# Performance work log

Measured on AMD Instinct MI355X. Metric: run time of the kernel, lower is better.

The kernel has to match this reference:

```python
import jax, jax.numpy as jnp
import numpy as np

B, S, E, H = 2, 2048, 512, 8
HD = E // H  # head dim = 64


def setup_inputs() -> dict:
    key = jax.random.key(0)
    k1, k2, k3 = jax.random.split(key, 3)
    scale_qkv = (6.0 / (E + 3 * E)) ** 0.5  # xavier-uniform-like scale
    scale_o = (6.0 / (E + E)) ** 0.5
    return {
        "X": jax.random.normal(k1, (B, S, E), dtype=jnp.float32),
        "Wqkv": jax.random.uniform(k2, (E, 3 * E), jnp.float32, -scale_qkv, scale_qkv),
        "bqkv": jnp.zeros((3 * E,), jnp.float32),
        "Wo": jax.random.uniform(k3, (E, E), jnp.float32, -scale_o, scale_o),
        "bo": jnp.zeros((E,), jnp.float32),
    }


def reference(X, Wqkv, bqkv, Wo, bo):
    b, s, e = X.shape
    # qkv projection: [B,S,3E] -> [B,S,H,3*HD] -> [B,H,S,3*HD]
    qkv = X @ Wqkv + bqkv
    qkv = qkv.reshape(b, s, H, 3 * HD).transpose(0, 2, 1, 3)
    q, k, v = jnp.array_split(qkv, 3, axis=-1)  # each [B,H,S,HD]
    # naive scaled dot-product attention (full score matrix, per source)
    attn_logits = jnp.einsum("bhqd,bhkd->bhqk", q, k) / jnp.sqrt(jnp.float32(HD))
    attention = jax.nn.softmax(attn_logits, axis=-1)  # [B,H,S,S]
    values = jnp.einsum("bhqk,bhkd->bhqd", attention, v)
    values = values.transpose(0, 2, 1, 3).reshape(b, s, e)
    o = values @ Wo + bo
    return (o, attention)
```

## Files before the change

### kernel.cpp

```cpp
#include <hip/hip_runtime.h>

typedef unsigned short u16;
typedef u16 u16x2 __attribute__((ext_vector_type(2)));
typedef u16 u16x4 __attribute__((ext_vector_type(4)));
typedef u16 u16x8 __attribute__((ext_vector_type(8)));
typedef __bf16 bf16x8 __attribute__((ext_vector_type(8)));
typedef float f32x4 __attribute__((ext_vector_type(4)));
typedef float f32x2 __attribute__((ext_vector_type(2)));

#define MFMA16(A, B, C) __builtin_amdgcn_mfma_f32_16x16x32_bf16(A, B, C, 0, 0, 0)

#define SB 2
#define SS 2048
#define SE 512
#define SH 8
#define SHD 64

__device__ __forceinline__ u16 f2b(float f) {
  union { float f; unsigned u; } v;
  v.f = f;
  unsigned r = v.u + 0x7FFFu + ((v.u >> 16) & 1u);
  return (u16)(r >> 16);
}

__device__ __forceinline__ bf16x8 as_bf16x8(u16x8 v) {
  return __builtin_bit_cast(bf16x8, v);
}

__global__ __launch_bounds__(256)
void convx_kernel(const float* __restrict__ X, u16* __restrict__ Xb)
{
  const int i = (blockIdx.x * 256 + threadIdx.x) * 4;
  const float4 v = *(const float4*)&X[i];
  u16x4 o;
  o[0] = f2b(v.x); o[1] = f2b(v.y); o[2] = f2b(v.z); o[3] = f2b(v.w);
  *(u16x4*)&Xb[i] = o;
}

__global__ __launch_bounds__(256)
void wtrans_kernel(const float* __restrict__ in, u16* __restrict__ out, int N)
{
  __shared__ float t[32][33];
  const int tid = threadIdx.x;
  const int r = tid >> 3, c4 = (tid & 7) * 4;
  const int k0 = blockIdx.y * 32, n0 = blockIdx.x * 32;
  const float4 v = *(const float4*)&in[(size_t)(k0 + r) * N + n0 + c4];
  t[r][c4 + 0] = v.x; t[r][c4 + 1] = v.y; t[r][c4 + 2] = v.z; t[r][c4 + 3] = v.w;
  __syncthreads();
  u16x4 o;
  o[0] = f2b(t[c4 + 0][r]);
  o[1] = f2b(t[c4 + 1][r]);
  o[2] = f2b(t[c4 + 2][r]);
  o[3] = f2b(t[c4 + 3][r]);
  *(u16x4*)&out[(n0 + r) * 512 + k0 + c4] = o;
}

template <int MODE>
__global__ __launch_bounds__(256, 2)
void gemm_kernel(const u16* __restrict__ A, const u16* __restrict__ Bt,
                 const float* __restrict__ bias,
                 u16* __restrict__ Q, u16* __restrict__ K, u16* __restrict__ Vt,
                 float* __restrict__ Out)
{
  __shared__ __align__(16) u16 As[128 * 40];
  __shared__ __align__(16) u16 Bs[128 * 40];
  const int tid  = threadIdx.x;
  const int lane = tid & 63, wave = tid >> 6, quad = lane >> 4, l16 = lane & 15;
  const int m0 = blockIdx.y * 128, n0 = blockIdx.x * 128;
  const int wr = (wave >> 1) * 64, wc = (wave & 1) * 64;
  const int sr = tid >> 2, sc = (tid & 3) * 8;

  const f32x4 z4 = {0.f, 0.f, 0.f, 0.f};
  f32x4 acc[4][4];
#pragma unroll
  for (int i = 0; i < 4; i++)
#pragma unroll
    for (int j = 0; j < 4; j++) acc[i][j] = z4;

  for (int k0 = 0; k0 < 512; k0 += 32) {
    const u16x8 a0 = *(const u16x8*)&A[(m0 + sr) * 512 + k0 + sc];
    const u16x8 a1 = *(const u16x8*)&A[(m0 + 64 + sr) * 512 + k0 + sc];
    const u16x8 b0 = *(const u16x8*)&Bt[(n0 + sr) * 512 + k0 + sc];
    const u16x8 b1 = *(const u16x8*)&Bt[(n0 + 64 + sr) * 512 + k0 + sc];
    __syncthreads();
    *(u16x8*)&As[sr * 40 + sc]        = a0;
    *(u16x8*)&As[(64 + sr) * 40 + sc] = a1;
    *(u16x8*)&Bs[sr * 40 + sc]        = b0;
    *(u16x8*)&Bs[(64 + sr) * 40 + sc] = b1;
    __syncthreads();
    bf16x8 af[4], bf[4];
#pragma unroll
    for (int i = 0; i < 4; i++) {
      af[i] = as_bf16x8(*(const u16x8*)&As[(wr + i * 16 + l16) * 40 + quad * 8]);
      bf[i] = as_bf16x8(*(const u16x8*)&Bs[(wc + i * 16 + l16) * 40 + quad * 8]);
    }
#pragma unroll
    for (int i = 0; i < 4; i++)
#pragma unroll
      for (int j = 0; j < 4; j++) acc[i][j] = MFMA16(af[i], bf[j], acc[i][j]);
  }

#pragma unroll
  for (int tm = 0; tm < 4; tm++) {
#pragma unroll
    for (int tn = 0; tn < 4; tn++) {
#pragma unroll
      for (int r = 0; r < 4; r++) {
        const int gm = m0 + wr + tm * 16 + quad * 4 + r;
        const int gn = n0 + wc + tn * 16 + l16;
        const float v = acc[tm][tn][r] + bias[gn];
        if (MODE == 0) {
          const int bb = gm >> 11, s = gm & 2047;
          const int hh = gn / 192, j = gn - hh * 192;
          const int bh = bb * SH + hh;
          if (j < 64)
            Q[(bh * SS + s) * SHD + j] = f2b(v * 0.125f);
          else if (j < 128)
            K[(bh * SS + s) * SHD + (j - 64)] = f2b(v);
          else
            Vt[(bh * SHD + (j - 128)) * SS + s] = f2b(v);
        } else {
          Out[gm * 512 + gn] = v;
        }
      }
    }
  }
}

__global__ __launch_bounds__(512, 2)
void attn_kernel(const u16* __restrict__ Q, const u16* __restrict__ K,
                 const u16* __restrict__ Vt, u16* __restrict__ values,
                 float* __restrict__ attn)
{
  __shared__ __align__(16) u16 p_lds[8 * 16 * 264];
  __shared__ float redmax[8][16];
  __shared__ float redsum[8][16];

  const int tid  = threadIdx.x;
  const int lane = tid & 63, wave = tid >> 6, quad = lane >> 4, l16 = lane & 15;
  const int q0 = blockIdx.x * 16;
  const int h = blockIdx.y, b = blockIdx.z, bh = b * SH + h;

  const u16* Qb = Q + bh * SS * SHD;
  const u16* Kb = K + bh * SS * SHD;
  const u16* Vb = Vt + bh * SHD * SS;

  const bf16x8 aq0 = as_bf16x8(*(const u16x8*)&Qb[(q0 + l16) * SHD + quad * 8]);
  const bf16x8 aq1 = as_bf16x8(*(const u16x8*)&Qb[(q0 + l16) * SHD + 32 + quad * 8]);

  f32x4 acc[16];
#pragma unroll
  for (int ct = 0; ct < 16; ct++) {
    const int kb = wave * 256 + ct * 16;
    bf16x8 bk0 = as_bf16x8(*(const u16x8*)&Kb[(kb + l16) * SHD + quad * 8]);
    bf16x8 bk1 = as_bf16x8(*(const u16x8*)&Kb[(kb + l16) * SHD + 32 + quad * 8]);
    f32x4 c = {0.f, 0.f, 0.f, 0.f};
    c = MFMA16(aq0, bk0, c);
    c = MFMA16(aq1, bk1, c);
    acc[ct] = c;
  }

  float mx[4];
#pragma unroll
  for (int r = 0; r < 4; r++) mx[r] = acc[0][r];
#pragma unroll
  for (int ct = 1; ct < 16; ct++)
#pragma unroll
    for (int r = 0; r < 4; r++) mx[r] = fmaxf(mx[r], acc[ct][r]);
#pragma unroll
  for (int off = 1; off < 16; off <<= 1)
#pragma unroll
    for (int r = 0; r < 4; r++) mx[r] = fmaxf(mx[r], __shfl_xor(mx[r], off));
  if (l16 == 0) {
#pragma unroll
    for (int r = 0; r < 4; r++) redmax[wave][quad * 4 + r] = mx[r];
  }
  __syncthreads();
  float gm[4];
#pragma unroll
  for (int r = 0; r < 4; r++) {
    float m = redmax[0][quad * 4 + r];
#pragma unroll
    for (int w = 1; w < 8; w++) m = fmaxf(m, redmax[w][quad * 4 + r]);
    gm[r] = m;
  }

  float ls[4] = {0.f, 0.f, 0.f, 0.f};
#pragma unroll
  for (int ct = 0; ct < 16; ct++)
#pragma unroll
    for (int r = 0; r < 4; r++) {
      const float p = __expf(acc[ct][r] - gm[r]);
      acc[ct][r] = p;
      ls[r] += p;
    }
#pragma unroll
  for (int off = 1; off < 16; off <<= 1)
#pragma unroll
    for (int r = 0; r < 4; r++) ls[r] += __shfl_xor(ls[r], off);
  if (l16 == 0) {
#pragma unroll
    for (int r = 0; r < 4; r++) redsum[wave][quad * 4 + r] = ls[r];
  }
  __syncthreads();
  float inv[4];
#pragma unroll
  for (int r = 0; r < 4; r++) {
    float s = redsum[0][quad * 4 + r];
#pragma unroll
    for (int w = 1; w < 8; w++) s += redsum[w][quad * 4 + r];
    inv[r] = 1.f / s;
  }

  float* attn_b = attn + (bh * SS + q0) * SS;
#pragma unroll
  for (int ct = 0; ct < 16; ct++) {
    const int col = wave * 256 + ct * 16 + l16;
#pragma unroll
    for (int r = 0; r < 4; r++) {
      const float p = acc[ct][r] * inv[r];
      attn_b[(quad * 4 + r) * SS + col] = p;
      p_lds[(wave * 16 + quad * 4 + r) * 264 + ct * 16 + l16] = f2b(p);
    }
  }

  f32x4 oacc[4];
#pragma unroll
  for (int nt = 0; nt < 4; nt++) oacc[nt] = (f32x4){0.f, 0.f, 0.f, 0.f};
#pragma unroll
  for (int kc = 0; kc < 8; kc++) {
    bf16x8 pa = as_bf16x8(*(const u16x8*)&p_lds[(wave * 16 + l16) * 264 + kc * 32 + quad * 8]);
    const int sb = wave * 256 + kc * 32 + quad * 8;
#pragma unroll
    for (int nt = 0; nt < 4; nt++) {
      bf16x8 vb = as_bf16x8(*(const u16x8*)&Vb[(nt * 16 + l16) * SS + sb]);
      oacc[nt] = MFMA16(pa, vb, oacc[nt]);
    }
  }

  __syncthreads();
  float* opart = (float*)p_lds;
#pragma unroll
  for (int nt = 0; nt < 4; nt++)
#pragma unroll
    for (int r = 0; r < 4; r++)
      opart[(wave * 16 + quad * 4 + r) * 64 + nt * 16 + l16] = oacc[nt][r];
  __syncthreads();

  const int q = tid >> 5, d0 = (tid & 31) * 2;
  f32x2 s2 = {0.f, 0.f};
#pragma unroll
  for (int w = 0; w < 8; w++) s2 += *(const f32x2*)&opart[(w * 16 + q) * 64 + d0];
  u16x2 o2;
  o2[0] = f2b(s2[0]);
  o2[1] = f2b(s2[1]);
  *(u16x2*)&values[((b * SS + q0 + q) * SH + h) * SHD + d0] = o2;
}

extern "C" void kernel_launch(void* const* d_in, const int* in_sizes, int n_in,
                              void* d_out, int out_size, void* d_ws, size_t ws_size,
                              hipStream_t stream) {
  const float* X    = (const float*)d_in[0];
  const float* Wqkv = (const float*)d_in[1];
  const float* bqkv = (const float*)d_in[2];
  const float* Wo   = (const float*)d_in[3];
  const float* bo   = (const float*)d_in[4];

  float* o_out    = (float*)d_out;
  float* attn_out = o_out + SB * SS * SE;

  const size_t QKV_ELEMS = (size_t)SB * SH * SS * SHD;
  u16* Q      = (u16*)d_ws;
  u16* K      = Q + QKV_ELEMS;
  u16* Vt     = K + QKV_ELEMS;
  u16* values = Vt + QKV_ELEMS;
  u16* Xb     = values;
  u16* WqkvT  = (u16*)attn_out;
  u16* WoT    = Q;

  convx_kernel<<<dim3(2048), 256, 0, stream>>>(X, Xb);
  wtrans_kernel<<<dim3(48, 16), 256, 0, stream>>>(Wqkv, WqkvT, 1536);

  gemm_kernel<0><<<dim3(12, 32), 256, 0, stream>>>(Xb, WqkvT, bqkv, Q, K, Vt, nullptr);
  attn_kernel<<<dim3(128, 8, 2), 512, 0, stream>>>(Q, K, Vt, values, attn_out);
  wtrans_kernel<<<dim3(16, 16), 256, 0, stream>>>(Wo, WoT, 512);
  gemm_kernel<1><<<dim3(4, 32), 256, 0, stream>>>(values, WoT, bo,
                                                  nullptr, nullptr, nullptr, o_out);
}
```

Measured before the change: 441.2 us.

## Restructure attention so each wave owns full query rows with two-pass online softmax

Each wave now handles 16 full query rows across all 2048 keys, instead of eight waves splitting the key range of one 16-row tile. It uses a first pass with online max/sum statistics and a second pass that recomputes QK^T to write probabilities and accumulate PV. This removes the cross-wave LDS reductions, block barriers and the partial-output reduction. The grid is remapped to 512 blocks of 256 threads with a swizzled block index for L2 locality, and the LDS stride is padded. The cost is recomputing QK^T twice and re-reading K per wave.

```diff
diff --git a/kernel.cpp b/kernel.cpp
--- a/kernel.cpp
+++ b/kernel.cpp
@@ -127,134 +127,122 @@
   }
 }
 
-__global__ __launch_bounds__(512, 2)
+#define PSTR 268
+
+__global__ __launch_bounds__(256, 2)
 void attn_kernel(const u16* __restrict__ Q, const u16* __restrict__ K,
                  const u16* __restrict__ Vt, u16* __restrict__ values,
                  float* __restrict__ attn)
 {
-  __shared__ __align__(16) u16 p_lds[8 * 16 * 264];
-  __shared__ float redmax[8][16];
-  __shared__ float redsum[8][16];
+  __shared__ __align__(16) u16 p_lds[4][16 * PSTR];
 
   const int tid  = threadIdx.x;
   const int lane = tid & 63, wave = tid >> 6, quad = lane >> 4, l16 = lane & 15;
-  const int q0 = blockIdx.x * 16;
-  const int h = blockIdx.y, b = blockIdx.z, bh = b * SH + h;
-
-  const u16* Qb = Q + bh * SS * SHD;
-  const u16* Kb = K + bh * SS * SHD;
-  const u16* Vb = Vt + bh * SHD * SS;
+
+  const int bid = blockIdx.x;
+  const int wg  = (bid & 7) * 64 + (bid >> 3);
+  const int qt  = wg & 31;
+  const int bh  = wg >> 5;
+  const int h = bh & 7, b = bh >> 3;
+  const int q0 = qt * 64 + wave * 16;
+
+  const u16* Qb = Q + (size_t)bh * SS * SHD;
+  const u16* Kb = K + (size_t)bh * SS * SHD;
+  const u16* Vb = Vt + (size_t)bh * SHD * SS;
 
   const bf16x8 aq0 = as_bf16x8(*(const u16x8*)&Qb[(q0 + l16) * SHD + quad * 8]);
   const bf16x8 aq1 = as_bf16x8(*(const u16x8*)&Qb[(q0 + l16) * SHD + 32 + quad * 8]);
 
-  f32x4 acc[16];
-#pragma unroll
-  for (int ct = 0; ct < 16; ct++) {
-    const int kb = wave * 256 + ct * 16;
-    bf16x8 bk0 = as_bf16x8(*(const u16x8*)&Kb[(kb + l16) * SHD + quad * 8]);
-    bf16x8 bk1 = as_bf16x8(*(const u16x8*)&Kb[(kb + l16) * SHD + 32 + quad * 8]);
-    f32x4 c = {0.f, 0.f, 0.f, 0.f};
-    c = MFMA16(aq0, bk0, c);
-    c = MFMA16(aq1, bk1, c);
-    acc[ct] = c;
-  }
-
-  float mx[4];
-#pragma unroll
-  for (int r = 0; r < 4; r++) mx[r] = acc[0][r];
-#pragma unroll
-  for (int ct = 1; ct < 16; ct++)
-#pragma unroll
-    for (int r = 0; r < 4; r++) mx[r] = fmaxf(mx[r], acc[ct][r]);
-#pragma unroll
-  for (int off = 1; off < 16; off <<= 1)
-#pragma unroll
-    for (int r = 0; r < 4; r++) mx[r] = fmaxf(mx[r], __shfl_xor(mx[r], off));
-  if (l16 == 0) {
-#pragma unroll
-    for (int r = 0; r < 4; r++) redmax[wave][quad * 4 + r] = mx[r];
-  }
-  __syncthreads();
-  float gm[4];
-#pragma unroll
-  for (int r = 0; r < 4; r++) {
-    float m = redmax[0][quad * 4 + r];
-#pragma unroll
-    for (int w = 1; w < 8; w++) m = fmaxf(m, redmax[w][quad * 4 + r]);
-    gm[r] = m;
-  }
-
-  float ls[4] = {0.f, 0.f, 0.f, 0.f};
-#pragma unroll
-  for (int ct = 0; ct < 16; ct++)
+  float m[4] = {-1e30f, -1e30f, -1e30f, -1e30f};
+  float l[4] = {0.f, 0.f, 0.f, 0.f};
+  for (int kt = 0; kt < 8; kt++) {
+    f32x4 acc[16];
+#pragma unroll
+    for (int ct = 0; ct < 16; ct++) {
+      const int kb = kt * 256 + ct * 16;
+      bf16x8 bk0 = as_bf16x8(*(const u16x8*)&Kb[(kb + l16) * SHD + quad * 8]);
+      bf16x8 bk1 = as_bf16x8(*(const u16x8*)&Kb[(kb + l16) * SHD + 32 + quad * 8]);
+      f32x4 c = {0.f, 0.f, 0.f, 0.f};
+      c = MFMA16(aq0, bk0, c);
+      c = MFMA16(aq1, bk1, c);
+      acc[ct] = c;
+    }
 #pragma unroll
     for (int r = 0; r < 4; r++) {
-      const float p = __expf(acc[ct][r] - gm[r]);
-      acc[ct][r] = p;
-      ls[r] += p;
-    }
-#pragma unroll
-  for (int off = 1; off < 16; off <<= 1)
-#pragma unroll
-    for (int r = 0; r < 4; r++) ls[r] += __shfl_xor(ls[r], off);
-  if (l16 == 0) {
-#pragma unroll
-    for (int r = 0; r < 4; r++) redsum[wave][quad * 4 + r] = ls[r];
-  }
-  __syncthreads();
+      float tm = acc[0][r];
+#pragma unroll
+      for (int ct = 1; ct < 16; ct++) tm = fmaxf(tm, acc[ct][r]);
+      const float mn = fmaxf(m[r], tm);
+      float s = 0.f;
+#pragma unroll
+      for (int ct = 0; ct < 16; ct++) s += __expf(acc[ct][r] - mn);
+      l[r] = l[r] * __expf(m[r] - mn) + s;
+      m[r] = mn;
+    }
+  }
+#pragma unroll
+  for (int off = 1; off < 16; off <<= 1) {
+#pragma unroll
+    for (int r = 0; r < 4; r++) {
+      const float m2 = __shfl_xor(m[r], off);
+      const float l2 = __shfl_xor(l[r], off);
+      const float mn = fmaxf(m[r], m2);
+      l[r] = l[r] * __expf(m[r] - mn) + l2 * __expf(m2 - mn);
+      m[r] = mn;
+    }
+  }
   float inv[4];
 #pragma unroll
-  for (int r = 0; r < 4; r++) {
-    float s = redsum[0][quad * 4 + r];
-#pragma unroll
-    for (int w = 1; w < 8; w++) s += redsum[w][quad * 4 + r];
-    inv[r] = 1.f / s;
-  }
-
-  float* attn_b = attn + (bh * SS + q0) * SS;
-#pragma unroll
-  for (int ct = 0; ct < 16; ct++) {
-    const int col = wave * 256 + ct * 16 + l16;
+  for (int r = 0; r < 4; r++) inv[r] = 1.f / l[r];
+
+  float* attn_b = attn + ((size_t)bh * SS + q0) * SS;
+  u16* pl = &p_lds[wave][0];
+  f32x4 oacc[4];
+#pragma unroll
+  for (int nt = 0; nt < 4; nt++) oacc[nt] = (f32x4){0.f, 0.f, 0.f, 0.f};
+
+  for (int kt = 0; kt < 8; kt++) {
+    f32x4 acc[16];
+#pragma unroll
+    for (int ct = 0; ct < 16; ct++) {
+      const int kb = kt * 256 + ct * 16;
+      bf16x8 bk0 = as_bf16x8(*(const u16x8*)&Kb[(kb + l16) * SHD + quad * 8]);
+      bf16x8 bk1 = as_bf16x8(*(const u16x8*)&Kb[(kb + l16) * SHD + 32 + quad * 8]);
+      f32x4 c = {0.f, 0.f, 0.f, 0.f};
+      c = MFMA16(aq0, bk0, c);
+      c = MFMA16(aq1, bk1, c);
+      acc[ct] = c;
+    }
+#pragma unroll
+    for (int ct = 0; ct < 16; ct++) {
+#pragma unroll
+      for (int r = 0; r < 4; r++) {
+        const float p = __expf(acc[ct][r] - m[r]) * inv[r];
+        attn_b[(quad * 4 + r) * SS + kt * 256 + ct * 16 + l16] = p;
+        pl[(quad * 4 + r) * PSTR + ct * 16 + l16] = f2b(p);
+      }
+    }
+#pragma unroll
+    for (int kc = 0; kc < 8; kc++) {
+      bf16x8 pa = as_bf16x8(*(const u16x8*)&pl[l16 * PSTR + kc * 32 + quad * 8]);
+      const int sb = kt * 256 + kc * 32 + quad * 8;
+#pragma unroll
+      for (int nt = 0; nt < 4; nt++) {
+        bf16x8 vb = as_bf16x8(*(const u16x8*)&Vb[(nt * 16 + l16) * SS + sb]);
+        oacc[nt] = MFMA16(pa, vb, oacc[nt]);
+      }
+    }
+  }
+
+#pragma unroll
+  for (int nt = 0; nt < 4; nt++) {
 #pragma unroll
     for (int r = 0; r < 4; r++) {
-      const float p = acc[ct][r] * inv[r];
-      attn_b[(quad * 4 + r) * SS + col] = p;
-      p_lds[(wave * 16 + quad * 4 + r) * 264 + ct * 16 + l16] = f2b(p);
-    }
-  }
-
-  f32x4 oacc[4];
-#pragma unroll
-  for (int nt = 0; nt < 4; nt++) oacc[nt] = (f32x4){0.f, 0.f, 0.f, 0.f};
-#pragma unroll
-  for (int kc = 0; kc < 8; kc++) {
-    bf16x8 pa = as_bf16x8(*(const u16x8*)&p_lds[(wave * 16 + l16) * 264 + kc * 32 + quad * 8]);
-    const int sb = wave * 256 + kc * 32 + quad * 8;
-#pragma unroll
-    for (int nt = 0; nt < 4; nt++) {
-      bf16x8 vb = as_bf16x8(*(const u16x8*)&Vb[(nt * 16 + l16) * SS + sb]);
-      oacc[nt] = MFMA16(pa, vb, oacc[nt]);
-    }
-  }
-
-  __syncthreads();
-  float* opart = (float*)p_lds;
-#pragma unroll
-  for (int nt = 0; nt < 4; nt++)
-#pragma unroll
-    for (int r = 0; r < 4; r++)
-      opart[(wave * 16 + quad * 4 + r) * 64 + nt * 16 + l16] = oacc[nt][r];
-  __syncthreads();
-
-  const int q = tid >> 5, d0 = (tid & 31) * 2;
-  f32x2 s2 = {0.f, 0.f};
-#pragma unroll
-  for (int w = 0; w < 8; w++) s2 += *(const f32x2*)&opart[(w * 16 + q) * 64 + d0];
-  u16x2 o2;
-  o2[0] = f2b(s2[0]);
-  o2[1] = f2b(s2[1]);
-  *(u16x2*)&values[((b * SS + q0 + q) * SH + h) * SHD + d0] = o2;
+      const int qrow = q0 + quad * 4 + r;
+      values[((size_t)(b * SS + qrow) * SH + h) * SHD + nt * 16 + l16] =
+          f2b(oacc[nt][r]);
+    }
+  }
 }
 
 extern "C" void kernel_launch(void* const* d_in, const int* in_sizes, int n_in,
@@ -282,7 +270,7 @@
   wtrans_kernel<<<dim3(48, 16), 256, 0, stream>>>(Wqkv, WqkvT, 1536);
 
   gemm_kernel<0><<<dim3(12, 32), 256, 0, stream>>>(Xb, WqkvT, bqkv, Q, K, Vt, nullptr);
-  attn_kernel<<<dim3(128, 8, 2), 512, 0, stream>>>(Q, K, Vt, values, attn_out);
+  attn_kernel<<<dim3(512), 256, 0, stream>>>(Q, K, Vt, values, attn_out);
   wtrans_kernel<<<dim3(16, 16), 256, 0, stream>>>(Wo, WoT, 512);
   gemm_kernel<1><<<dim3(4, 32), 256, 0, stream>>>(values, WoT, bo,
                                                   nullptr, nullptr, nullptr, o_out);
```

After: 474.7 us. 7.6% more time.

## Merge softmax max/sum reductions into one barrier with rescaling, nontemporal attn stores

Applied to the files above, without the earlier changes.

Each wave now computes a local max and local sum of exponentials before a single block barrier. The global max and sum are then combined online with exp rescaling, which replaces the previous two-barrier max-then-sum sequence. Per-wave LDS regions let the barrier before the partial-output writes be dropped, and the attention matrix is written with nontemporal stores to avoid polluting cache. Launch bounds are raised to 4 blocks per CU to push occupancy, which risks register spills since each thread holds 16 accumulator vectors.

```diff
diff --git a/kernel.cpp b/kernel.cpp
--- a/kernel.cpp
+++ b/kernel.cpp
@@ -127,23 +127,26 @@
   }
 }
 
-__global__ __launch_bounds__(512, 2)
+#define PSTR 264
+#define PWAVE (16 * PSTR)
+
+__global__ __launch_bounds__(512, 4)
 void attn_kernel(const u16* __restrict__ Q, const u16* __restrict__ K,
                  const u16* __restrict__ Vt, u16* __restrict__ values,
                  float* __restrict__ attn)
 {
-  __shared__ __align__(16) u16 p_lds[8 * 16 * 264];
-  __shared__ float redmax[8][16];
-  __shared__ float redsum[8][16];
+  __shared__ __align__(16) u16 p_lds[8 * PWAVE];
+  __shared__ float srm[8][16];
+  __shared__ float srl[8][16];
 
   const int tid  = threadIdx.x;
   const int lane = tid & 63, wave = tid >> 6, quad = lane >> 4, l16 = lane & 15;
   const int q0 = blockIdx.x * 16;
   const int h = blockIdx.y, b = blockIdx.z, bh = b * SH + h;
 
-  const u16* Qb = Q + bh * SS * SHD;
-  const u16* Kb = K + bh * SS * SHD;
-  const u16* Vb = Vt + bh * SHD * SS;
+  const u16* Qb = Q + (size_t)bh * SS * SHD;
+  const u16* Kb = K + (size_t)bh * SS * SHD;
+  const u16* Vb = Vt + (size_t)bh * SHD * SS;
 
   const bf16x8 aq0 = as_bf16x8(*(const u16x8*)&Qb[(q0 + l16) * SHD + quad * 8]);
   const bf16x8 aq1 = as_bf16x8(*(const u16x8*)&Qb[(q0 + l16) * SHD + 32 + quad * 8]);
@@ -160,67 +163,61 @@
     acc[ct] = c;
   }
 
-  float mx[4];
-#pragma unroll
-  for (int r = 0; r < 4; r++) mx[r] = acc[0][r];
-#pragma unroll
-  for (int ct = 1; ct < 16; ct++)
-#pragma unroll
-    for (int r = 0; r < 4; r++) mx[r] = fmaxf(mx[r], acc[ct][r]);
-#pragma unroll
-  for (int off = 1; off < 16; off <<= 1)
-#pragma unroll
-    for (int r = 0; r < 4; r++) mx[r] = fmaxf(mx[r], __shfl_xor(mx[r], off));
+  float mw[4], lw[4];
+#pragma unroll
+  for (int r = 0; r < 4; r++) {
+    float m = acc[0][r];
+#pragma unroll
+    for (int ct = 1; ct < 16; ct++) m = fmaxf(m, acc[ct][r]);
+#pragma unroll
+    for (int off = 1; off < 16; off <<= 1) m = fmaxf(m, __shfl_xor(m, off));
+    mw[r] = m;
+  }
+#pragma unroll
+  for (int r = 0; r < 4; r++) {
+    float s = 0.f;
+#pragma unroll
+    for (int ct = 0; ct < 16; ct++) {
+      const float p = __expf(acc[ct][r] - mw[r]);
+      acc[ct][r] = p;
+      s += p;
+    }
+#pragma unroll
+    for (int off = 1; off < 16; off <<= 1) s += __shfl_xor(s, off);
+    lw[r] = s;
+  }
   if (l16 == 0) {
 #pragma unroll
-    for (int r = 0; r < 4; r++) redmax[wave][quad * 4 + r] = mx[r];
+    for (int r = 0; r < 4; r++) {
+      srm[wave][quad * 4 + r] = mw[r];
+      srl[wave][quad * 4 + r] = lw[r];
+    }
   }
   __syncthreads();
-  float gm[4];
+
+  float scale[4];
 #pragma unroll
   for (int r = 0; r < 4; r++) {
-    float m = redmax[0][quad * 4 + r];
-#pragma unroll
-    for (int w = 1; w < 8; w++) m = fmaxf(m, redmax[w][quad * 4 + r]);
-    gm[r] = m;
-  }
-
-  float ls[4] = {0.f, 0.f, 0.f, 0.f};
-#pragma unroll
-  for (int ct = 0; ct < 16; ct++)
-#pragma unroll
-    for (int r = 0; r < 4; r++) {
-      const float p = __expf(acc[ct][r] - gm[r]);
-      acc[ct][r] = p;
-      ls[r] += p;
-    }
-#pragma unroll
-  for (int off = 1; off < 16; off <<= 1)
-#pragma unroll
-    for (int r = 0; r < 4; r++) ls[r] += __shfl_xor(ls[r], off);
-  if (l16 == 0) {
-#pragma unroll
-    for (int r = 0; r < 4; r++) redsum[wave][quad * 4 + r] = ls[r];
-  }
-  __syncthreads();
-  float inv[4];
-#pragma unroll
-  for (int r = 0; r < 4; r++) {
-    float s = redsum[0][quad * 4 + r];
-#pragma unroll
-    for (int w = 1; w < 8; w++) s += redsum[w][quad * 4 + r];
-    inv[r] = 1.f / s;
-  }
-
-  float* attn_b = attn + (bh * SS + q0) * SS;
+    const int row = quad * 4 + r;
+    float mg = srm[0][row];
+#pragma unroll
+    for (int w = 1; w < 8; w++) mg = fmaxf(mg, srm[w][row]);
+    float lg = 0.f;
+#pragma unroll
+    for (int w = 0; w < 8; w++) lg += srl[w][row] * __expf(srm[w][row] - mg);
+    scale[r] = __expf(mw[r] - mg) / lg;
+  }
+
+  float* attn_b = attn + ((size_t)bh * SS + q0) * SS;
+  u16* pl = &p_lds[wave * PWAVE];
 #pragma unroll
   for (int ct = 0; ct < 16; ct++) {
     const int col = wave * 256 + ct * 16 + l16;
 #pragma unroll
     for (int r = 0; r < 4; r++) {
-      const float p = acc[ct][r] * inv[r];
-      attn_b[(quad * 4 + r) * SS + col] = p;
-      p_lds[(wave * 16 + quad * 4 + r) * 264 + ct * 16 + l16] = f2b(p);
+      const float p = acc[ct][r] * scale[r];
+      __builtin_nontemporal_store(p, &attn_b[(quad * 4 + r) * SS + col]);
+      pl[(quad * 4 + r) * PSTR + ct * 16 + l16] = f2b(p);
     }
   }
 
@@ -229,7 +226,7 @@
   for (int nt = 0; nt < 4; nt++) oacc[nt] = (f32x4){0.f, 0.f, 0.f, 0.f};
 #pragma unroll
   for (int kc = 0; kc < 8; kc++) {
-    bf16x8 pa = as_bf16x8(*(const u16x8*)&p_lds[(wave * 16 + l16) * 264 + kc * 32 + quad * 8]);
+    bf16x8 pa = as_bf16x8(*(const u16x8*)&pl[l16 * PSTR + kc * 32 + quad * 8]);
     const int sb = wave * 256 + kc * 32 + quad * 8;
 #pragma unroll
     for (int nt = 0; nt < 4; nt++) {
@@ -238,23 +235,25 @@
     }
   }
 
-  __syncthreads();
-  float* opart = (float*)p_lds;
+  float* op = (float*)pl;
 #pragma unroll
   for (int nt = 0; nt < 4; nt++)
 #pragma unroll
     for (int r = 0; r < 4; r++)
-      opart[(wave * 16 + quad * 4 + r) * 64 + nt * 16 + l16] = oacc[nt][r];
+      op[(quad * 4 + r) * 64 + nt * 16 + l16] = oacc[nt][r];
   __syncthreads();
 
   const int q = tid >> 5, d0 = (tid & 31) * 2;
   f32x2 s2 = {0.f, 0.f};
 #pragma unroll
-  for (int w = 0; w < 8; w++) s2 += *(const f32x2*)&opart[(w * 16 + q) * 64 + d0];
+  for (int w = 0; w < 8; w++) {
+    const float* opw = (const float*)&p_lds[w * PWAVE];
+    s2 += *(const f32x2*)&opw[q * 64 + d0];
+  }
   u16x2 o2;
   o2[0] = f2b(s2[0]);
   o2[1] = f2b(s2[1]);
-  *(u16x2*)&values[((b * SS + q0 + q) * SH + h) * SHD + d0] = o2;
+  *(u16x2*)&values[((size_t)(b * SS + q0 + q) * SH + h) * SHD + d0] = o2;
 }
 
 extern "C" void kernel_launch(void* const* d_in, const int* in_sizes, int n_in,
```

Result: faster. 425.7 us (-3.5%).
